# Kernel tuning notes

Measured on AMD Instinct MI355X. Metric: run time of the kernel, lower is better.

The kernel has to match this reference:

```python
import jax, jax.numpy as jnp
import numpy as np

N = 30000      # num nodes
E = 600000     # num edges
D = 128        # feature dim (all layers)
R = 7          # num_relation
G = 16         # num graphs in batch
L = 3          # num layers (hidden_dims = [128,128,128])


def setup_inputs() -> dict:
    key = jax.random.key(0)
    ks = jax.random.split(key, 10)
    x = jax.random.normal(ks[0], (N, D), dtype=jnp.float32)
    node_in = jax.random.randint(ks[1], (E,), 0, N)
    node_out = jax.random.randint(ks[2], (E,), 0, N)
    relation = jax.random.randint(ks[3], (E,), 0, R)
    edge_weight = jax.random.uniform(ks[4], (E,), dtype=jnp.float32)
    node2graph = jnp.sort(jax.random.randint(ks[5], (N,), 0, G))
    # learned params: per-layer relational linear (R*D -> D) and self-loop linear (D -> D)
    Wr = jax.random.normal(ks[6], (L, R * D, D), dtype=jnp.float32) * 0.02
    br = jnp.zeros((L, D), dtype=jnp.float32)
    Wl = jax.random.normal(ks[7], (L, D, D), dtype=jnp.float32) * 0.02
    bl = jnp.zeros((L, D), dtype=jnp.float32)
    return dict(x=x, node_in=node_in, node_out=node_out, relation=relation,
                edge_weight=edge_weight, node2graph=node2graph,
                Wr=Wr, br=br, Wl=Wl, bl=bl)


def reference(x, node_in, node_out, relation, edge_weight, node2graph, Wr, br, Wl, bl):
    # relation-indexed destination segment: node_out * R + relation
    seg = node_out * R + relation            # (E,)
    ew = edge_weight[:, None]                # (E, 1)
    h = x
    for i in range(L):
        msg = h[node_in] * ew                                         # gather + weight, (E, D)
        upd = jax.ops.segment_sum(msg, seg, num_segments=N * R)       # scatter_add, (N*R, D)
        upd = upd.reshape(N, R * D)                                   # per-relation concat
        h = jax.nn.relu(upd @ Wr[i] + br[i] + h @ Wl[i] + bl[i])      # linear + self-loop + act
    node_feature = h                                                  # (N, D)
    graph_feature = jax.ops.segment_sum(node_feature, node2graph, num_segments=G)  # sum readout
    return graph_feature, node_feature
```

## Files before the change

### kernel.cpp

```cpp
#include <hip/hip_runtime.h>
#include <hip/hip_bf16.h>

#define NN 30000
#define NE 600000
#define DD 128
#define RR 7
#define GG 16
#define LL 3

#define NB64 ((NN + 63) / 64)

typedef short bf16x8 __attribute__((ext_vector_type(8)));
typedef float f32x4  __attribute__((ext_vector_type(4)));

__device__ __forceinline__ unsigned short f2bf(float f) {
    unsigned u = __float_as_uint(f);
    unsigned r = (u + 0x7fffu + ((u >> 16) & 1u)) >> 16;
    return (unsigned short)r;
}
__device__ __forceinline__ float bf2f(unsigned short b) {
    return __uint_as_float(((unsigned)b) << 16);
}
__device__ __forceinline__ ushort2 pk2bf(float a, float b) {
    __hip_bfloat162 t = __float22bfloat162_rn(make_float2(a, b));
    return *(ushort2*)&t;
}

__device__ __forceinline__ void gl_lds16(const void* g, void* l) {
    __builtin_amdgcn_global_load_lds(
        (const __attribute__((address_space(1))) void*)g,
        (__attribute__((address_space(3))) void*)l, 16, 0, 0);
}

__global__ __launch_bounds__(256) void pack_weights(
    const float* __restrict__ Wl,
    const float* __restrict__ Wr,
    unsigned short* __restrict__ Bw)
{
    int t = blockIdx.x * 256 + threadIdx.x;
    if (t >= LL * 1024 * DD) return;
    int l = t >> 17;
    int rem = t & 131071;
    int n = rem >> 7;
    int k = rem & 127;
    float v;
    if (n < DD) {
        v = Wl[(size_t)l * DD * DD + k * DD + n];
    } else {
        int q = n - DD;
        v = Wr[(size_t)l * RR * DD * DD + (size_t)((q >> 7) * DD + k) * DD + (q & 127)];
    }
    Bw[(size_t)l * 1024 * DD + n * DD + k] = f2bf(v);
}

__global__ __launch_bounds__(256) void convert_bf16(
    const float* __restrict__ in, unsigned short* __restrict__ out, int n4)
{
    int i = blockIdx.x * 256 + threadIdx.x;
    if (i >= n4) return;
    float4 v = ((const float4*)in)[i];
    ushort2 lo = pk2bf(v.x, v.y);
    ushort2 hi = pk2bf(v.z, v.w);
    ((ushort4*)out)[i] = make_ushort4(lo.x, lo.y, hi.x, hi.y);
}

__global__ __launch_bounds__(256) void bucket_hist(
    const int* __restrict__ node_out, int* __restrict__ bcnt, int E)
{
    int e = blockIdx.x * 256 + threadIdx.x;
    if (e < E) atomicAdd(&bcnt[(node_out[e] >> 6) * 16], 1);
}

__global__ __launch_bounds__(512) void bucket_scan(
    const int* __restrict__ bcnt, int* __restrict__ bstart,
    int* __restrict__ bcur, int nb)
{
    __shared__ int s[512];
    int t = threadIdx.x;
    int v = (t < nb) ? bcnt[t * 16] : 0;
    s[t] = v;
    __syncthreads();
#pragma unroll
    for (int off = 1; off < 512; off <<= 1) {
        int u = (t >= off) ? s[t - off] : 0;
        __syncthreads();
        s[t] += u;
        __syncthreads();
    }
    if (t <= nb) {
        int excl = s[t] - v;
        bstart[t] = excl;
        if (t < nb) bcur[t * 16] = excl;
    }
}

__global__ __launch_bounds__(256) void bucket_scatter(
    const int* __restrict__ node_in,
    const int* __restrict__ node_out,
    const int* __restrict__ relation,
    const float* __restrict__ ew,
    int* __restrict__ bcur,
    int2* __restrict__ tmp,
    int E)
{
    int e = blockIdx.x * 256 + threadIdx.x;
    if (e >= E) return;
    int o = node_out[e];
    int pos = atomicAdd(&bcur[(o >> 6) * 16], 1);
    tmp[pos] = make_int2(((o & 63) << 18) | (node_in[e] << 3) | relation[e],
                         __float_as_int(ew[e]));
}

__global__ __launch_bounds__(256) void bucket_sort(
    const int2* __restrict__ tmp,
    const int* __restrict__ bstart,
    int2* __restrict__ meta,
    int* __restrict__ start,
    int N)
{
    __shared__ int hist[64];
    __shared__ int scan[64];
    __shared__ int cur[64];
    const int b = blockIdx.x;
    const int t = threadIdx.x;
    const int s0 = bstart[b];
    const int s1 = bstart[b + 1];

    if (t < 64) hist[t] = 0;
    __syncthreads();
    for (int i = s0 + t; i < s1; i += 256)
        atomicAdd(&hist[((unsigned)tmp[i].x) >> 18], 1);
    __syncthreads();

    int v = (t < 64) ? hist[t] : 0;
    if (t < 64) scan[t] = v;
    __syncthreads();
#pragma unroll
    for (int off = 1; off < 64; off <<= 1) {
        int u = (t < 64 && t >= off) ? scan[t - off] : 0;
        __syncthreads();
        if (t < 64) scan[t] += u;
        __syncthreads();
    }
    if (t < 64) {
        int excl = scan[t] - v;
        cur[t] = s0 + excl;
        int node = b * 64 + t;
        if (node <= N) start[node] = s0 + excl;
    }
    __syncthreads();

    for (int i = s0 + t; i < s1; i += 256) {
        int2 m = tmp[i];
        int j = ((unsigned)m.x) >> 18;
        int pos = atomicAdd(&cur[j], 1);
        int key = m.x & 0x3ffff;
        int in = key >> 3, rel = key & 7;
        meta[pos] = make_int2((in * RR + rel) << 7, m.y);
    }
}

__global__ __launch_bounds__(256) void gemm_mfma(
    const unsigned short* __restrict__ hb,
    const unsigned short* __restrict__ Bw,
    const float* __restrict__ br,
    const float* __restrict__ bl,
    unsigned short* __restrict__ haccb,
    unsigned short* __restrict__ Zb,
    int N)
{
    __shared__ unsigned short As[64 * 128];
    __shared__ unsigned short Bs[256 * 128];

    const int tid  = threadIdx.x;
    const int wave = tid >> 6;
    const int lane = tid & 63;
    const int quad = lane >> 4;
    const int l16  = lane & 15;
    const int row0 = blockIdx.x * 64;
    const int col0 = blockIdx.y * 256;

    const int lr = lane >> 4;
    const int ls = lane & 15;

#pragma unroll
    for (int i = 0; i < 4; ++i) {
        int g = i * 4 + wave;
        int r = g * 4 + lr;
        int slot = ls ^ (r & 7);
        gl_lds16(hb + (size_t)(row0 + r) * 128 + slot * 8, As + g * 512);
    }
#pragma unroll
    for (int i = 0; i < 16; ++i) {
        int g = i * 4 + wave;
        int r = g * 4 + lr;
        int slot = ls ^ (r & 7);
        gl_lds16(Bw + (size_t)(col0 + r) * 128 + slot * 8, Bs + g * 512);
    }
    __syncthreads();

    f32x4 acc[4][4];
#pragma unroll
    for (int mt = 0; mt < 4; ++mt)
#pragma unroll
        for (int nt = 0; nt < 4; ++nt)
            acc[mt][nt] = (f32x4){0.f, 0.f, 0.f, 0.f};

    const unsigned short* As_l = As + l16 * 128;
    const unsigned short* Bs_l = Bs + (wave * 64 + l16) * 128;
    const int swz = l16 & 7;

#pragma unroll
    for (int kc = 0; kc < 4; ++kc) {
        int so = ((kc * 4 + quad) ^ swz) * 8;
        bf16x8 a0 = *(const bf16x8*)(As_l + 0 * 16 * 128 + so);
        bf16x8 a1 = *(const bf16x8*)(As_l + 1 * 16 * 128 + so);
        bf16x8 a2 = *(const bf16x8*)(As_l + 2 * 16 * 128 + so);
        bf16x8 a3 = *(const bf16x8*)(As_l + 3 * 16 * 128 + so);
        bf16x8 b0 = *(const bf16x8*)(Bs_l + 0 * 16 * 128 + so);
        bf16x8 b1 = *(const bf16x8*)(Bs_l + 1 * 16 * 128 + so);
        bf16x8 b2 = *(const bf16x8*)(Bs_l + 2 * 16 * 128 + so);
        bf16x8 b3 = *(const bf16x8*)(Bs_l + 3 * 16 * 128 + so);
#pragma unroll
        for (int mt = 0; mt < 4; ++mt) {
            bf16x8 a = (mt == 0) ? a0 : (mt == 1) ? a1 : (mt == 2) ? a2 : a3;
            acc[mt][0] = __builtin_amdgcn_mfma_f32_16x16x32_bf16(a, b0, acc[mt][0], 0, 0, 0);
            acc[mt][1] = __builtin_amdgcn_mfma_f32_16x16x32_bf16(a, b1, acc[mt][1], 0, 0, 0);
            acc[mt][2] = __builtin_amdgcn_mfma_f32_16x16x32_bf16(a, b2, acc[mt][2], 0, 0, 0);
            acc[mt][3] = __builtin_amdgcn_mfma_f32_16x16x32_bf16(a, b3, acc[mt][3], 0, 0, 0);
        }
    }

    if (col0 == 0 && wave < 2) {
        float bias[4];
#pragma unroll
        for (int nt = 0; nt < 4; ++nt) {
            int c = wave * 64 + nt * 16 + l16;
            bias[nt] = br[c] + bl[c];
        }
#pragma unroll
        for (int mt = 0; mt < 4; ++mt) {
#pragma unroll
            for (int reg = 0; reg < 4; ++reg) {
                int row = row0 + mt * 16 + quad * 4 + reg;
                if (row < N) {
                    ushort2 p01 = pk2bf(acc[mt][0][reg] + bias[0],
                                        acc[mt][1][reg] + bias[1]);
                    ushort2 p23 = pk2bf(acc[mt][2][reg] + bias[2],
                                        acc[mt][3][reg] + bias[3]);
                    unsigned short* dst = haccb + (size_t)row * 128 + wave * 64 + l16;
                    dst[0]  = p01.x;
                    dst[16] = p01.y;
                    dst[32] = p23.x;
                    dst[48] = p23.y;
                }
            }
        }
    } else {
        const int zc = col0 + wave * 64 - 128;
#pragma unroll
        for (int mt = 0; mt < 4; ++mt) {
#pragma unroll
            for (int reg = 0; reg < 4; ++reg) {
                int row = row0 + mt * 16 + quad * 4 + reg;
                if (row < N) {
                    ushort2 p01 = pk2bf(acc[mt][0][reg], acc[mt][1][reg]);
                    ushort2 p23 = pk2bf(acc[mt][2][reg], acc[mt][3][reg]);
                    unsigned short* dst = Zb + (size_t)row * (RR * DD) + zc + l16;
                    dst[0]  = p01.x;
                    dst[16] = p01.y;
                    dst[32] = p23.x;
                    dst[48] = p23.y;
                }
            }
        }
    }
}

__global__ __launch_bounds__(256) void aggregate(
    const unsigned short* __restrict__ Zb,
    const int* __restrict__ start,
    const int2* __restrict__ meta,
    const unsigned short* __restrict__ haccb,
    float* __restrict__ out_f32,
    unsigned short* __restrict__ out_bf16,
    int N)
{
    int wid = (blockIdx.x * 256 + threadIdx.x) >> 6;
    int lane = threadIdx.x & 63;
    if (wid >= N) return;

    const int grp  = lane >> 4;
    const int l16  = lane & 15;
    const int base = l16 * 8;

    int e0 = start[wid];
    int e1 = start[wid + 1];

    float acc[8];
#pragma unroll
    for (int k = 0; k < 8; ++k) acc[k] = 0.f;

    for (int eb = e0; eb < e1; eb += 64) {
        int2 mm = make_int2(0, 0);
        if (eb + lane < e1) mm = meta[eb + lane];
        int cnt = e1 - eb; if (cnt > 64) cnt = 64;
        for (int j = 0; j < cnt; j += 4) {
            int idx = j + grp;
            int key = __shfl(mm.x, idx, 64);
            float wt = __uint_as_float((unsigned)__shfl(mm.y, idx, 64));
            uint4 u = *(const uint4*)(Zb + (size_t)(unsigned)key + base);
            acc[0] = fmaf(wt, __uint_as_float(u.x << 16),          acc[0]);
            acc[1] = fmaf(wt, __uint_as_float(u.x & 0xffff0000u),  acc[1]);
            acc[2] = fmaf(wt, __uint_as_float(u.y << 16),          acc[2]);
            acc[3] = fmaf(wt, __uint_as_float(u.y & 0xffff0000u),  acc[3]);
            acc[4] = fmaf(wt, __uint_as_float(u.z << 16),          acc[4]);
            acc[5] = fmaf(wt, __uint_as_float(u.z & 0xffff0000u),  acc[5]);
            acc[6] = fmaf(wt, __uint_as_float(u.w << 16),          acc[6]);
            acc[7] = fmaf(wt, __uint_as_float(u.w & 0xffff0000u),  acc[7]);
        }
    }

#pragma unroll
    for (int k = 0; k < 8; ++k) {
        acc[k] += __shfl_xor(acc[k], 16, 64);
        acc[k] += __shfl_xor(acc[k], 32, 64);
    }

    uint4 hb4 = *(const uint4*)(haccb + (size_t)wid * DD + base);
    float o[8];
    o[0] = fmaxf(__uint_as_float(hb4.x << 16)         + acc[0], 0.f);
    o[1] = fmaxf(__uint_as_float(hb4.x & 0xffff0000u) + acc[1], 0.f);
    o[2] = fmaxf(__uint_as_float(hb4.y << 16)         + acc[2], 0.f);
    o[3] = fmaxf(__uint_as_float(hb4.y & 0xffff0000u) + acc[3], 0.f);
    o[4] = fmaxf(__uint_as_float(hb4.z << 16)         + acc[4], 0.f);
    o[5] = fmaxf(__uint_as_float(hb4.z & 0xffff0000u) + acc[5], 0.f);
    o[6] = fmaxf(__uint_as_float(hb4.w << 16)         + acc[6], 0.f);
    o[7] = fmaxf(__uint_as_float(hb4.w & 0xffff0000u) + acc[7], 0.f);

    if (grp == 0) {
        if (out_f32) {
            float* dst = out_f32 + (size_t)wid * DD + base;
            *(float4*)(dst)     = make_float4(o[0], o[1], o[2], o[3]);
            *(float4*)(dst + 4) = make_float4(o[4], o[5], o[6], o[7]);
        }
        if (out_bf16) {
            ushort2 p0 = pk2bf(o[0], o[1]);
            ushort2 p1 = pk2bf(o[2], o[3]);
            ushort2 p2 = pk2bf(o[4], o[5]);
            ushort2 p3 = pk2bf(o[6], o[7]);
            uint4 ub;
            ub.x = (unsigned)p0.x | ((unsigned)p0.y << 16);
            ub.y = (unsigned)p1.x | ((unsigned)p1.y << 16);
            ub.z = (unsigned)p2.x | ((unsigned)p2.y << 16);
            ub.w = (unsigned)p3.x | ((unsigned)p3.y << 16);
            *(uint4*)(out_bf16 + (size_t)wid * DD + base) = ub;
        }
    }
}

__global__ __launch_bounds__(256) void graph_sum(
    const float* __restrict__ nf,
    const int* __restrict__ n2g,
    float* __restrict__ gf,
    int N)
{
    int t = blockIdx.x * 256 + threadIdx.x;
    int chunk = t >> 5;
    int lane = t & 31;
    int n0 = chunk * 16;
    if (n0 >= N) return;
    int nend = n0 + 16; if (nend > N) nend = N;

    float4 acc = make_float4(0.f, 0.f, 0.f, 0.f);
    int curg = n2g[n0];
    for (int n = n0; n < nend; ++n) {
        int g = n2g[n];
        if (g != curg) {
            float* dst = gf + (size_t)curg * DD + lane * 4;
            atomicAdd(dst + 0, acc.x); atomicAdd(dst + 1, acc.y);
            atomicAdd(dst + 2, acc.z); atomicAdd(dst + 3, acc.w);
            acc = make_float4(0.f, 0.f, 0.f, 0.f);
            curg = g;
        }
        float4 v = *(const float4*)(nf + (size_t)n * DD + lane * 4);
        acc.x += v.x; acc.y += v.y; acc.z += v.z; acc.w += v.w;
    }
    float* dst = gf + (size_t)curg * DD + lane * 4;
    atomicAdd(dst + 0, acc.x); atomicAdd(dst + 1, acc.y);
    atomicAdd(dst + 2, acc.z); atomicAdd(dst + 3, acc.w);
}

extern "C" void kernel_launch(void* const* d_in, const int* in_sizes, int n_in,
                              void* d_out, int out_size, void* d_ws, size_t ws_size,
                              hipStream_t stream)
{
    const float* x        = (const float*)d_in[0];
    const int*   node_in  = (const int*)d_in[1];
    const int*   node_out = (const int*)d_in[2];
    const int*   relation = (const int*)d_in[3];
    const float* ew       = (const float*)d_in[4];
    const int*   n2g      = (const int*)d_in[5];
    const float* Wr       = (const float*)d_in[6];
    const float* br       = (const float*)d_in[7];
    const float* Wl       = (const float*)d_in[8];
    const float* bl       = (const float*)d_in[9];

    float* out = (float*)d_out;
    float* gf = out;
    float* nf = out + GG * DD;

    char* w = (char*)d_ws;
    unsigned short* Zb   = (unsigned short*)w; w += (size_t)NN * RR * DD * 2;
    unsigned short* haccb= (unsigned short*)w; w += (size_t)NN * DD * 2;
    unsigned short* hbA  = (unsigned short*)w; w += (size_t)NN * DD * 2;
    unsigned short* hbB  = (unsigned short*)w; w += (size_t)NN * DD * 2;
    unsigned short* Bw   = (unsigned short*)w; w += (size_t)LL * 1024 * DD * 2;
    int2*  meta   = (int2*)w;                  w += (size_t)NE * 8;
    int2*  tmp    = (int2*)w;                  w += (size_t)NE * 8;
    int*   start  = (int*)w;                   w += (size_t)(NN + 1) * 4 + 60;
    int*   bcnt   = (int*)w;                   w += (size_t)NB64 * 16 * 4 + 64;
    int*   bcur   = (int*)w;                   w += (size_t)NB64 * 16 * 4 + 64;
    int*   bstart = (int*)w;                   w += (size_t)(NB64 + 1) * 4 + 60;

    const int N = NN, E = NE;

    pack_weights<<<(LL * 1024 * DD + 255) / 256, 256, 0, stream>>>(Wl, Wr, Bw);
    convert_bf16<<<(N * DD / 4 + 255) / 256, 256, 0, stream>>>(x, hbA, N * DD / 4);

    hipMemsetAsync(bcnt, 0, (size_t)NB64 * 16 * sizeof(int), stream);
    bucket_hist<<<(E + 255) / 256, 256, 0, stream>>>(node_out, bcnt, E);
    bucket_scan<<<1, 512, 0, stream>>>(bcnt, bstart, bcur, NB64);
    bucket_scatter<<<(E + 255) / 256, 256, 0, stream>>>(
        node_in, node_out, relation, ew, bcur, tmp, E);
    bucket_sort<<<NB64, 256, 0, stream>>>(tmp, bstart, meta, start, N);

    dim3 ggrid((N + 63) / 64, 4);
    unsigned short* hin = hbA;
    unsigned short* hnext = hbB;
    for (int l = 0; l < LL; ++l) {
        const float* br_l = br + (size_t)l * DD;
        const float* bl_l = bl + (size_t)l * DD;
        const unsigned short* Bw_l = Bw + (size_t)l * 1024 * DD;

        gemm_mfma<<<ggrid, 256, 0, stream>>>(hin, Bw_l, br_l, bl_l, haccb, Zb, N);

        bool last = (l == LL - 1);
        aggregate<<<(N * 64 + 255) / 256, 256, 0, stream>>>(
            Zb, start, meta, haccb,
            last ? nf : (float*)nullptr,
            last ? (unsigned short*)nullptr : hnext, N);

        unsigned short* t = hin; hin = hnext; hnext = t;
    }

    hipMemsetAsync(gf, 0, (size_t)GG * DD * sizeof(float), stream);
    int chunks = (N + 15) / 16;
    graph_sum<<<(chunks * 32 + 255) / 256, 256, 0, stream>>>(nf, n2g, gf, N);
}
```

Before: 329.5 us.

## Store per-relation transformed features as FP8 with permuted channel layout

The per-relation projection Zb written by the GEMM and gathered per edge in aggregate is now stored as FP8 (e4m3 via cvt_pk_fp8) instead of bf16. This halves the bytes of the dominant random gather traffic. The channel order is also permuted consistently across weight packing, input conversion, epilogue stores and final output, so each lane writes contiguous packed values. The cost is a large precision drop in the messages, which risks exceeding accuracy tolerance.

```diff
diff --git a/kernel.cpp b/kernel.cpp
--- a/kernel.cpp
+++ b/kernel.cpp
@@ -12,14 +12,13 @@
 
 typedef short bf16x8 __attribute__((ext_vector_type(8)));
 typedef float f32x4  __attribute__((ext_vector_type(4)));
+typedef float f32x2  __attribute__((ext_vector_type(2)));
+
 
 __device__ __forceinline__ unsigned short f2bf(float f) {
     unsigned u = __float_as_uint(f);
     unsigned r = (u + 0x7fffu + ((u >> 16) & 1u)) >> 16;
     return (unsigned short)r;
-}
-__device__ __forceinline__ float bf2f(unsigned short b) {
-    return __uint_as_float(((unsigned)b) << 16);
 }
 __device__ __forceinline__ ushort2 pk2bf(float a, float b) {
     __hip_bfloat162 t = __float22bfloat162_rn(make_float2(a, b));
@@ -42,7 +41,9 @@
     int l = t >> 17;
     int rem = t & 131071;
     int n = rem >> 7;
-    int k = rem & 127;
+    int k_pos = rem & 127;
+    int kp = k_pos & 63;
+    int k = (k_pos & ~63) + (kp & 3) * 16 + (kp >> 2);
     float v;
     if (n < DD) {
         v = Wl[(size_t)l * DD * DD + k * DD + n];
@@ -50,18 +51,22 @@
         int q = n - DD;
         v = Wr[(size_t)l * RR * DD * DD + (size_t)((q >> 7) * DD + k) * DD + (q & 127)];
     }
-    Bw[(size_t)l * 1024 * DD + n * DD + k] = f2bf(v);
+    Bw[t] = f2bf(v);
 }
 
 __global__ __launch_bounds__(256) void convert_bf16(
-    const float* __restrict__ in, unsigned short* __restrict__ out, int n4)
-{
-    int i = blockIdx.x * 256 + threadIdx.x;
-    if (i >= n4) return;
-    float4 v = ((const float4*)in)[i];
-    ushort2 lo = pk2bf(v.x, v.y);
-    ushort2 hi = pk2bf(v.z, v.w);
-    ((ushort4*)out)[i] = make_ushort4(lo.x, lo.y, hi.x, hi.y);
+    const float* __restrict__ in, unsigned short* __restrict__ out, int n32)
+{
+    int t = blockIdx.x * 256 + threadIdx.x;
+    if (t >= n32) return;
+    int row = t >> 5;
+    int pg  = t & 31;
+    int span = pg >> 4;
+    int q = pg & 15;
+    const float* xr = in + (size_t)row * DD + span * 64 + q;
+    ushort2 a = pk2bf(xr[0],  xr[16]);
+    ushort2 b = pk2bf(xr[32], xr[48]);
+    ((ushort4*)out)[t] = make_ushort4(a.x, a.y, b.x, b.y);
 }
 
 __global__ __launch_bounds__(256) void bucket_hist(
@@ -166,7 +171,7 @@
     const float* __restrict__ br,
     const float* __restrict__ bl,
     unsigned short* __restrict__ haccb,
-    unsigned short* __restrict__ Zb,
+    unsigned char* __restrict__ Zb8,
     int N)
 {
     __shared__ unsigned short As[64 * 128];
@@ -248,29 +253,24 @@
                                         acc[mt][1][reg] + bias[1]);
                     ushort2 p23 = pk2bf(acc[mt][2][reg] + bias[2],
                                         acc[mt][3][reg] + bias[3]);
-                    unsigned short* dst = haccb + (size_t)row * 128 + wave * 64 + l16;
-                    dst[0]  = p01.x;
-                    dst[16] = p01.y;
-                    dst[32] = p23.x;
-                    dst[48] = p23.y;
+                    *(ushort4*)(haccb + (size_t)row * 128 + wave * 64 + l16 * 4) =
+                        make_ushort4(p01.x, p01.y, p23.x, p23.y);
                 }
             }
         }
     } else {
-        const int zc = col0 + wave * 64 - 128;
+        const int zpos = col0 + wave * 64 - 128;
 #pragma unroll
         for (int mt = 0; mt < 4; ++mt) {
 #pragma unroll
             for (int reg = 0; reg < 4; ++reg) {
                 int row = row0 + mt * 16 + quad * 4 + reg;
                 if (row < N) {
-                    ushort2 p01 = pk2bf(acc[mt][0][reg], acc[mt][1][reg]);
-                    ushort2 p23 = pk2bf(acc[mt][2][reg], acc[mt][3][reg]);
-                    unsigned short* dst = Zb + (size_t)row * (RR * DD) + zc + l16;
-                    dst[0]  = p01.x;
-                    dst[16] = p01.y;
-                    dst[32] = p23.x;
-                    dst[48] = p23.y;
+                    int u = __builtin_amdgcn_cvt_pk_fp8_f32(
+                        acc[mt][0][reg], acc[mt][1][reg], 0, false);
+                    u = __builtin_amdgcn_cvt_pk_fp8_f32(
+                        acc[mt][2][reg], acc[mt][3][reg], u, true);
+                    *(int*)(Zb8 + (size_t)row * (RR * DD) + zpos + l16 * 4) = u;
                 }
             }
         }
@@ -278,7 +278,7 @@
 }
 
 __global__ __launch_bounds__(256) void aggregate(
-    const unsigned short* __restrict__ Zb,
+    const unsigned char* __restrict__ Zb8,
     const int* __restrict__ start,
     const int2* __restrict__ meta,
     const unsigned short* __restrict__ haccb,
@@ -309,15 +309,19 @@
             int idx = j + grp;
             int key = __shfl(mm.x, idx, 64);
             float wt = __uint_as_float((unsigned)__shfl(mm.y, idx, 64));
-            uint4 u = *(const uint4*)(Zb + (size_t)(unsigned)key + base);
-            acc[0] = fmaf(wt, __uint_as_float(u.x << 16),          acc[0]);
-            acc[1] = fmaf(wt, __uint_as_float(u.x & 0xffff0000u),  acc[1]);
-            acc[2] = fmaf(wt, __uint_as_float(u.y << 16),          acc[2]);
-            acc[3] = fmaf(wt, __uint_as_float(u.y & 0xffff0000u),  acc[3]);
-            acc[4] = fmaf(wt, __uint_as_float(u.z << 16),          acc[4]);
-            acc[5] = fmaf(wt, __uint_as_float(u.z & 0xffff0000u),  acc[5]);
-            acc[6] = fmaf(wt, __uint_as_float(u.w << 16),          acc[6]);
-            acc[7] = fmaf(wt, __uint_as_float(u.w & 0xffff0000u),  acc[7]);
+            uint2 u = *(const uint2*)(Zb8 + (size_t)(unsigned)key + base);
+            f32x2 d0 = __builtin_amdgcn_cvt_pk_f32_fp8(u.x, false);
+            f32x2 d1 = __builtin_amdgcn_cvt_pk_f32_fp8(u.x, true);
+            f32x2 d2 = __builtin_amdgcn_cvt_pk_f32_fp8(u.y, false);
+            f32x2 d3 = __builtin_amdgcn_cvt_pk_f32_fp8(u.y, true);
+            acc[0] = fmaf(wt, d0[0], acc[0]);
+            acc[1] = fmaf(wt, d0[1], acc[1]);
+            acc[2] = fmaf(wt, d1[0], acc[2]);
+            acc[3] = fmaf(wt, d1[1], acc[3]);
+            acc[4] = fmaf(wt, d2[0], acc[4]);
+            acc[5] = fmaf(wt, d2[1], acc[5]);
+            acc[6] = fmaf(wt, d3[0], acc[6]);
+            acc[7] = fmaf(wt, d3[1], acc[7]);
         }
     }
 
@@ -339,11 +343,6 @@
     o[7] = fmaxf(__uint_as_float(hb4.w & 0xffff0000u) + acc[7], 0.f);
 
     if (grp == 0) {
-        if (out_f32) {
-            float* dst = out_f32 + (size_t)wid * DD + base;
-            *(float4*)(dst)     = make_float4(o[0], o[1], o[2], o[3]);
-            *(float4*)(dst + 4) = make_float4(o[4], o[5], o[6], o[7]);
-        }
         if (out_bf16) {
             ushort2 p0 = pk2bf(o[0], o[1]);
             ushort2 p1 = pk2bf(o[2], o[3]);
@@ -356,6 +355,14 @@
             ub.w = (unsigned)p3.x | ((unsigned)p3.y << 16);
             *(uint4*)(out_bf16 + (size_t)wid * DD + base) = ub;
         }
+        if (out_f32) {
+            int cb = ((l16 >> 3) << 6) + ((l16 & 7) << 1);
+            float* dst = out_f32 + (size_t)wid * DD;
+#pragma unroll
+            for (int j = 0; j < 4; ++j) {
+                *(float2*)(dst + cb + j * 16) = make_float2(o[j], o[j + 4]);
+            }
+        }
     }
 }
 
@@ -411,7 +418,7 @@
     float* nf = out + GG * DD;
 
     char* w = (char*)d_ws;
-    unsigned short* Zb   = (unsigned short*)w; w += (size_t)NN * RR * DD * 2;
+    unsigned char*  Zb8  = (unsigned char*)w;  w += (size_t)NN * RR * DD;
     unsigned short* haccb= (unsigned short*)w; w += (size_t)NN * DD * 2;
     unsigned short* hbA  = (unsigned short*)w; w += (size_t)NN * DD * 2;
     unsigned short* hbB  = (unsigned short*)w; w += (size_t)NN * DD * 2;
@@ -426,7 +433,7 @@
     const int N = NN, E = NE;
 
     pack_weights<<<(LL * 1024 * DD + 255) / 256, 256, 0, stream>>>(Wl, Wr, Bw);
-    convert_bf16<<<(N * DD / 4 + 255) / 256, 256, 0, stream>>>(x, hbA, N * DD / 4);
+    convert_bf16<<<(N * 32 + 255) / 256, 256, 0, stream>>>(x, hbA, N * 32);
 
     hipMemsetAsync(bcnt, 0, (size_t)NB64 * 16 * sizeof(int), stream);
     bucket_hist<<<(E + 255) / 256, 256, 0, stream>>>(node_out, bcnt, E);
@@ -443,11 +450,11 @@
         const float* bl_l = bl + (size_t)l * DD;
         const unsigned short* Bw_l = Bw + (size_t)l * 1024 * DD;
 
-        gemm_mfma<<<ggrid, 256, 0, stream>>>(hin, Bw_l, br_l, bl_l, haccb, Zb, N);
+        gemm_mfma<<<ggrid, 256, 0, stream>>>(hin, Bw_l, br_l, bl_l, haccb, Zb8, N);
 
         bool last = (l == LL - 1);
         aggregate<<<(N * 64 + 255) / 256, 256, 0, stream>>>(
-            Zb, start, meta, haccb,
+            Zb8, start, meta, haccb,
             last ? nf : (float*)nullptr,
             last ? (unsigned short*)nullptr : hnext, N);
 
```

New measurement: 297.9 us. 1.11x faster.
